# Optimization experiments

Measured on AMD Instinct MI355X. Metric: run time of the kernel, lower is better.

The kernel has to match this reference:

```python
import jax, jax.numpy as jnp
import numpy as np

B, S, H, E, T, L = 128, 1024, 512, 512, 64, 128


def setup_inputs() -> dict:
    key = jax.random.key(0)
    ks = jax.random.split(key, 20)
    s = 0.02
    inp = {
        "sent_lengths": jax.random.randint(ks[0], (B,), 1, S, dtype=jnp.int32),
        "output_length": T,
        "decoder_input": jax.random.normal(ks[1], (B, E), jnp.float32),
        "h0": jax.random.normal(ks[2], (B, H), jnp.float32),
        "c0": jax.random.normal(ks[3], (B, H), jnp.float32),
        "context": jax.random.normal(ks[4], (B, S, H), jnp.float32),
        "cur_labels": jax.random.randint(ks[5], (B, T), 0, L, dtype=jnp.int32),
        "cur_max_nsymbs": jax.random.randint(ks[6], (B,), 0, 10, dtype=jnp.int32),
        # parameters
        "label_emb": jax.random.normal(ks[7], (L, E), jnp.float32) * s,
        "W_ih": jax.random.normal(ks[8], (4 * H, E), jnp.float32) * s,
        "b_ih": jnp.zeros((4 * H,), jnp.float32),
        "W_hh": jax.random.normal(ks[9], (4 * H, H), jnp.float32) * s,
        "b_hh": jnp.zeros((4 * H,), jnp.float32),
        "W_ho": jax.random.normal(ks[10], (H, 2 * H), jnp.float32) * s,
        "b_ho": jnp.zeros((H,), jnp.float32),
        "W_attn_in": jax.random.normal(ks[11], (H, H), jnp.float32) * s,
        "b_attn_in": jnp.zeros((H,), jnp.float32),
        "W_attn_ctx": jax.random.normal(ks[12], (H, H), jnp.float32) * s,
        "b_attn_ctx": jnp.zeros((H,), jnp.float32),
        "V": jax.random.uniform(ks[13], (H,), jnp.float32, -1.0, 1.0),
        "W_out": jax.random.normal(ks[14], (L, 2 * H + E), jnp.float32) * s,
        "b_out": jnp.zeros((L,), jnp.float32),
    }
    # padding_idx row of the label embedding is zero (torch nn.Embedding semantics)
    inp["label_emb"] = inp["label_emb"].at[0].set(0.0)
    return inp


def _decode(output_length, decoder_input, h0, c0, context, cur_labels,
            label_emb, W_ih, b_ih, W_hh, b_hh, W_ho, b_ho,
            W_attn_in, b_attn_in, W_attn_ctx, b_attn_ctx, V, W_out, b_out):
    # Precompute the 1x1-conv context projection once (identical math to per-step conv).
    ctx = jnp.einsum("bsh,gh->bsg", context, W_attn_ctx) + b_attn_ctx  # [B,S,H]

    # Teacher-forced input sequence: x_0 = decoder_input, x_i = emb(labels[:, i-1]).
    emb = label_emb[cur_labels]                     # [B,T,E]
    xs = jnp.concatenate(
        [decoder_input[None], jnp.swapaxes(emb, 0, 1)[: output_length - 1]], axis=0
    )                                               # [T,B,E]

    def step(carry, x):
        h, c = carry
        gates = x @ W_ih.T + b_ih + h @ W_hh.T + b_hh          # [B,4H]
        i_g, f_g, g_g, o_g = jnp.split(gates, 4, axis=1)
        c_t = jax.nn.sigmoid(f_g) * c + jax.nn.sigmoid(i_g) * jnp.tanh(g_g)
        h_lstm = jax.nn.sigmoid(o_g) * jnp.tanh(c_t)            # [B,H]
        # pointer attention
        inp = h_lstm @ W_attn_in.T + b_attn_in                  # [B,H]
        att = jnp.einsum("bsh,h->bs", jnp.tanh(inp[:, None, :] + ctx), V)
        alpha = jax.nn.softmax(att, axis=-1)                    # [B,S]
        weighted = jnp.einsum("bs,bsh->bh", alpha, ctx)         # [B,H]
        hidden_t = jnp.tanh(jnp.concatenate([weighted, h_lstm], 1) @ W_ho.T + b_ho)
        out = jnp.concatenate([hidden_t, weighted, x], 1) @ W_out.T + b_out  # [B,L]
        return (hidden_t, c_t), out

    (h_f, c_f), outs = jax.lax.scan(step, (h0, c0), xs)  # outs [T,B,L]
    outputs = jnp.transpose(outs, (1, 0, 2))             # [B,T,L]
    preds = jnp.argmax(outputs, axis=-1)                 # [B,T]
    return outputs, preds, h_f, c_f


def reference(sent_lengths, output_length, decoder_input, h0, c0, context,
              cur_labels, cur_max_nsymbs, label_emb, W_ih, b_ih, W_hh, b_hh,
              W_ho, b_ho, W_attn_in, b_attn_in, W_attn_ctx, b_attn_ctx, V,
              W_out, b_out):
    # cur_batch_len = len(sent_lengths) == B, so hidden slicing is a no-op here.
    # cur_max_nsymbs unused (constrained_decoding=None path).
    return _decode(output_length, decoder_input, h0, c0, context, cur_labels,
                   label_emb, W_ih, b_ih, W_hh, b_hh, W_ho, b_ho,
                   W_attn_in, b_attn_in, W_attn_ctx, b_attn_ctx, V, W_out, b_out)
```

## Files before the change

### kernel.cpp

```cpp
#include <hip/hip_runtime.h>
#include <hip/hip_bf16.h>
#include <math.h>

#define B_ 128
#define S_ 1024
#define H_ 512
#define E_ 512
#define T_ 64
#define L_ 128
#define G4H 2048

__device__ inline float sigmoidf_(float x) { return 1.f / (1.f + expf(-x)); }
__device__ inline float fast_tanhf_(float x) {
    float e = __expf(2.f * x);
    return 1.f - 2.f / (e + 1.f);
}

__global__ __launch_bounds__(256) void gemm128(
    const float* __restrict__ A, int lda,
    const float* __restrict__ W, int ldw,
    const float* __restrict__ bias,
    const float* __restrict__ Cinit, int ldci,
    float* __restrict__ C, int ldc,
    int K, int act, int perm)
{
    __shared__ float As[16][128];
    __shared__ float Ws[16][128];
    const int m0 = blockIdx.x * 128;
    const int n0 = blockIdx.y * 128;
    const int t = threadIdx.x;
    const int tx = t & 15;
    const int ty = t >> 4;
    const int lr = t >> 1;
    const int lk = (t & 1) * 8;

    float acc[8][8] = {};

    for (int k0 = 0; k0 < K; k0 += 16) {
        float4 a0 = *reinterpret_cast<const float4*>(A + (size_t)(m0 + lr) * lda + k0 + lk);
        float4 a1 = *reinterpret_cast<const float4*>(A + (size_t)(m0 + lr) * lda + k0 + lk + 4);
        float4 w0 = *reinterpret_cast<const float4*>(W + (size_t)(n0 + lr) * ldw + k0 + lk);
        float4 w1 = *reinterpret_cast<const float4*>(W + (size_t)(n0 + lr) * ldw + k0 + lk + 4);
        As[lk + 0][lr] = a0.x; As[lk + 1][lr] = a0.y; As[lk + 2][lr] = a0.z; As[lk + 3][lr] = a0.w;
        As[lk + 4][lr] = a1.x; As[lk + 5][lr] = a1.y; As[lk + 6][lr] = a1.z; As[lk + 7][lr] = a1.w;
        Ws[lk + 0][lr] = w0.x; Ws[lk + 1][lr] = w0.y; Ws[lk + 2][lr] = w0.z; Ws[lk + 3][lr] = w0.w;
        Ws[lk + 4][lr] = w1.x; Ws[lk + 5][lr] = w1.y; Ws[lk + 6][lr] = w1.z; Ws[lk + 7][lr] = w1.w;
        __syncthreads();
#pragma unroll
        for (int kk = 0; kk < 16; ++kk) {
            float a[8], b[8];
#pragma unroll
            for (int i = 0; i < 8; ++i) a[i] = As[kk][ty * 8 + i];
#pragma unroll
            for (int j = 0; j < 8; ++j) b[j] = Ws[kk][tx * 8 + j];
#pragma unroll
            for (int i = 0; i < 8; ++i)
#pragma unroll
                for (int j = 0; j < 8; ++j) acc[i][j] = fmaf(a[i], b[j], acc[i][j]);
        }
        __syncthreads();
    }

#pragma unroll
    for (int i = 0; i < 8; ++i) {
        const int m = m0 + ty * 8 + i;
        size_t crow;
        if (perm) { int bb = m & 127, tt = m >> 7; crow = ((size_t)bb * T_ + tt) * ldc; }
        else crow = (size_t)m * ldc;
#pragma unroll
        for (int j = 0; j < 8; ++j) {
            const int n = n0 + tx * 8 + j;
            float v = acc[i][j];
            if (bias)  v += bias[n];
            if (Cinit) v += Cinit[(size_t)m * ldci + n];
            if (act == 1) v = tanhf(v);
            C[crow + n] = v;
        }
    }
}

__global__ __launch_bounds__(256) void gemm_stepk(
    const float* __restrict__ A, int lda,
    const float* __restrict__ W, int ldw,
    float* __restrict__ P, int N, int Kc)
{
    __shared__ float As[16][128];
    __shared__ float Ws[16][64];
    const int n0 = blockIdx.x * 64;
    const int k0 = blockIdx.y * Kc;
    const int t = threadIdx.x;
    const int tx = t & 15;
    const int ty = t >> 4;
    const int ar = t >> 1, akq = (t & 1) * 8;
    const int wr = t >> 2, wkq = (t & 3) * 4;

    float acc[8][4] = {};

    for (int kb = 0; kb < Kc; kb += 16) {
        float4 a0 = *reinterpret_cast<const float4*>(A + (size_t)ar * lda + k0 + kb + akq);
        float4 a1 = *reinterpret_cast<const float4*>(A + (size_t)ar * lda + k0 + kb + akq + 4);
        float4 w0 = *reinterpret_cast<const float4*>(W + (size_t)(n0 + wr) * ldw + k0 + kb + wkq);
        As[akq + 0][ar] = a0.x; As[akq + 1][ar] = a0.y; As[akq + 2][ar] = a0.z; As[akq + 3][ar] = a0.w;
        As[akq + 4][ar] = a1.x; As[akq + 5][ar] = a1.y; As[akq + 6][ar] = a1.z; As[akq + 7][ar] = a1.w;
        Ws[wkq + 0][wr] = w0.x; Ws[wkq + 1][wr] = w0.y; Ws[wkq + 2][wr] = w0.z; Ws[wkq + 3][wr] = w0.w;
        __syncthreads();
#pragma unroll
        for (int kk = 0; kk < 16; ++kk) {
            float a[8], b[4];
#pragma unroll
            for (int i = 0; i < 8; ++i) a[i] = As[kk][ty * 8 + i];
#pragma unroll
            for (int j = 0; j < 4; ++j) b[j] = Ws[kk][tx * 4 + j];
#pragma unroll
            for (int i = 0; i < 8; ++i)
#pragma unroll
                for (int j = 0; j < 4; ++j) acc[i][j] = fmaf(a[i], b[j], acc[i][j]);
        }
        __syncthreads();
    }

#pragma unroll
    for (int i = 0; i < 8; ++i) {
        const int m = ty * 8 + i;
#pragma unroll
        for (int j = 0; j < 4; ++j)
            P[((size_t)blockIdx.y * 128 + m) * N + n0 + tx * 4 + j] = acc[i][j];
    }
}

__global__ void k_embed(const float* __restrict__ dec_in, const int* __restrict__ labels,
                        const float* __restrict__ emb, float* __restrict__ X)
{
    size_t total = (size_t)T_ * B_ * E_;
    for (size_t i = (size_t)blockIdx.x * blockDim.x + threadIdx.x; i < total;
         i += (size_t)gridDim.x * blockDim.x) {
        int e = (int)(i % E_);
        int b = (int)((i / E_) % B_);
        int t = (int)(i / ((size_t)E_ * B_));
        float v;
        if (t == 0) v = dec_in[b * E_ + e];
        else {
            int lab = labels[b * T_ + (t - 1)];
            v = emb[(size_t)lab * E_ + e];
        }
        X[i] = v;
    }
}

__global__ void k_init(const float* __restrict__ h0, const float* __restrict__ c0,
                       const float* __restrict__ b_ih, const float* __restrict__ b_hh,
                       float* __restrict__ hbuf, float* __restrict__ cbuf, float* __restrict__ bsum)
{
    int i = blockIdx.x * blockDim.x + threadIdx.x;
    hbuf[i] = h0[i];
    cbuf[i] = c0[i];
    if (i < G4H) bsum[i] = b_ih[i] + b_hh[i];
}

__global__ __launch_bounds__(256) void k_lstm(const float* __restrict__ Pg,
                                              const float* __restrict__ xproj_t,
                                              float* __restrict__ cbuf, float* __restrict__ cat1)
{
    int i = blockIdx.x * blockDim.x + threadIdx.x;
    int b = i >> 9, h = i & 511;
    const float* p0 = Pg + (size_t)b * G4H;
    const float* p1 = Pg + (size_t)(128 + b) * G4H;
    const float* xp = xproj_t + (size_t)b * G4H;
    float ig = sigmoidf_(p0[h] + p1[h] + xp[h]);
    float fg = sigmoidf_(p0[h + 512] + p1[h + 512] + xp[h + 512]);
    float gg = tanhf(p0[h + 1024] + p1[h + 1024] + xp[h + 1024]);
    float og = sigmoidf_(p0[h + 1536] + p1[h + 1536] + xp[h + 1536]);
    float c = fg * cbuf[i] + ig * gg;
    cbuf[i] = c;
    cat1[b * 1024 + 512 + h] = og * tanhf(c);
}

__global__ __launch_bounds__(512) void k_attn(const float* __restrict__ ctx,
    const float* __restrict__ Pa, const float* __restrict__ b_ain,
    const float* __restrict__ Vv,
    float* __restrict__ pm, float* __restrict__ pl, float* __restrict__ pw)
{
    int blk = blockIdx.x;
    int b = blk >> 2, q = blk & 3;
    int tid = threadIdx.x, lane = tid & 63, wv = tid >> 6;

    __shared__ float inp_sh[512];
    inp_sh[tid] = Pa[(size_t)b * 512 + tid]
                + Pa[(size_t)(128 + b) * 512 + tid]
                + Pa[(size_t)(256 + b) * 512 + tid]
                + Pa[(size_t)(384 + b) * 512 + tid]
                + b_ain[tid];
    __syncthreads();

    float inpr[8], vr[8];
    {
        const float4* v4 = reinterpret_cast<const float4*>(Vv) + lane * 2;
        *(float4*)&vr[0] = v4[0];   *(float4*)&vr[4] = v4[1];
#pragma unroll
        for (int k = 0; k < 8; ++k) inpr[k] = inp_sh[lane * 8 + k];
    }
    const float* cbase = ctx + (size_t)b * S_ * H_ + (size_t)(q * 256) * H_;

    float m = -INFINITY, l = 0.f, w[8] = {};
    for (int si = 0; si < 32; ++si) {
        int s = wv * 32 + si;
        const float4* cp = reinterpret_cast<const float4*>(cbase + (size_t)s * H_) + lane * 2;
        float c8[8];
        *(float4*)&c8[0] = cp[0]; *(float4*)&c8[4] = cp[1];
        float t = 0.f;
#pragma unroll
        for (int k = 0; k < 8; ++k) t = fmaf(fast_tanhf_(inpr[k] + c8[k]), vr[k], t);
#pragma unroll
        for (int off = 32; off > 0; off >>= 1) t += __shfl_xor(t, off);
        float mn = fmaxf(m, t);
        float sc = __expf(m - mn);
        float p  = __expf(t - mn);
        l = l * sc + p;
#pragma unroll
        for (int k = 0; k < 8; ++k) w[k] = w[k] * sc + p * c8[k];
        m = mn;
    }

    __shared__ float wl[8 * 512];
    __shared__ float ml[8], ll[8];
#pragma unroll
    for (int k = 0; k < 8; ++k) wl[wv * 512 + lane * 8 + k] = w[k];
    if (lane == 0) { ml[wv] = m; ll[wv] = l; }
    __syncthreads();

    float M = ml[0];
#pragma unroll
    for (int u = 1; u < 8; ++u) M = fmaxf(M, ml[u]);
    float lt = 0.f, wt = 0.f;
#pragma unroll
    for (int u = 0; u < 8; ++u) {
        float e = __expf(ml[u] - M);
        lt += e * ll[u];
        wt += e * wl[u * 512 + tid];
    }
    if (tid == 0) { pm[blk] = M; pl[blk] = lt; }
    pw[(size_t)blk * 512 + tid] = wt;
}

__global__ __launch_bounds__(512) void k_merge(const float* __restrict__ pm,
    const float* __restrict__ pl, const float* __restrict__ pw,
    float* __restrict__ cat1, float* __restrict__ hist_t)
{
    int b = blockIdx.x, h = threadIdx.x;
    float M = -INFINITY;
#pragma unroll
    for (int q = 0; q < 4; ++q) M = fmaxf(M, pm[4 * b + q]);
    float L = 0.f, wt = 0.f;
#pragma unroll
    for (int q = 0; q < 4; ++q) {
        float e = __expf(pm[4 * b + q] - M);
        L += e * pl[4 * b + q];
        wt += e * pw[(size_t)(4 * b + q) * 512 + h];
    }
    float wv = wt / L;
    cat1[b * 1024 + h] = wv;
    hist_t[(size_t)b * 1024 + 512 + h] = wv;
}

__global__ __launch_bounds__(256) void k_whofin(const float* __restrict__ Po,
    const float* __restrict__ b_ho, float* __restrict__ hbuf, float* __restrict__ hist_t)
{
    int i = blockIdx.x * blockDim.x + threadIdx.x;
    int b = i >> 9, h = i & 511;
    float v = b_ho[h];
#pragma unroll
    for (int ks = 0; ks < 8; ++ks) v += Po[((size_t)ks * 128 + b) * 512 + h];
    v = tanhf(v);
    hbuf[i] = v;
    hist_t[(size_t)b * 1024 + h] = v;
}

__global__ __launch_bounds__(128) void k_argmax(const float* __restrict__ outp,
                                                float* __restrict__ preds)
{
    int row = blockIdx.x;
    int tid = threadIdx.x;
    float v = outp[(size_t)row * L_ + tid];
    int idx = tid;
#pragma unroll
    for (int off = 32; off > 0; off >>= 1) {
        float ov = __shfl_xor(v, off);
        int oi = __shfl_xor(idx, off);
        if (ov > v || (ov == v && oi < idx)) { v = ov; idx = oi; }
    }
    __shared__ float sv[2];
    __shared__ int si[2];
    if ((tid & 63) == 0) { sv[tid >> 6] = v; si[tid >> 6] = idx; }
    __syncthreads();
    if (tid == 0) {
        float v0 = sv[0], v1 = sv[1];
        int i0 = si[0], i1 = si[1];
        int r = (v1 > v0 || (v1 == v0 && i1 < i0)) ? i1 : i0;
        preds[row] = (float)r;
    }
}

__global__ void k_final(const float* __restrict__ hbuf, const float* __restrict__ cbuf,
                        float* __restrict__ hf, float* __restrict__ cf)
{
    int i = blockIdx.x * blockDim.x + threadIdx.x;
    hf[i] = hbuf[i];
    cf[i] = cbuf[i];
}

extern "C" void kernel_launch(void* const* d_in, const int* in_sizes, int n_in,
                              void* d_out, int out_size, void* d_ws, size_t ws_size,
                              hipStream_t stream)
{
    const float* dec_in  = (const float*)d_in[2];
    const float* h0      = (const float*)d_in[3];
    const float* c0      = (const float*)d_in[4];
    const float* context = (const float*)d_in[5];
    const int*   labels  = (const int*)d_in[6];
    const float* emb     = (const float*)d_in[8];
    const float* W_ih    = (const float*)d_in[9];
    const float* b_ih    = (const float*)d_in[10];
    const float* W_hh    = (const float*)d_in[11];
    const float* b_hh    = (const float*)d_in[12];
    const float* W_ho    = (const float*)d_in[13];
    const float* b_ho    = (const float*)d_in[14];
    const float* W_ain   = (const float*)d_in[15];
    const float* b_ain   = (const float*)d_in[16];
    const float* W_actx  = (const float*)d_in[17];
    const float* b_actx  = (const float*)d_in[18];
    const float* Vv      = (const float*)d_in[19];
    const float* W_out   = (const float*)d_in[20];
    const float* b_out   = (const float*)d_in[21];

    float* ws = (float*)d_ws;
    float* X     = ws; ws += (size_t)T_ * B_ * E_;
    float* xproj = ws; ws += (size_t)T_ * B_ * G4H;
    float* xout  = ws; ws += (size_t)T_ * B_ * L_;
    float* ctx   = ws; ws += (size_t)B_ * S_ * H_;
    float* hist  = ws; ws += (size_t)T_ * B_ * 1024;
    float* Pg    = ws; ws += (size_t)2 * B_ * G4H;
    float* Pa    = ws; ws += (size_t)4 * B_ * H_;
    float* Po    = ws; ws += (size_t)8 * B_ * H_;
    float* cbuf  = ws; ws += (size_t)B_ * H_;
    float* cat1  = ws; ws += (size_t)B_ * 1024;
    float* hbuf  = ws; ws += (size_t)B_ * H_;
    float* pm    = ws; ws += 512;
    float* pl    = ws; ws += 512;
    float* pw    = ws; ws += (size_t)512 * 512;
    float* bsum  = ws; ws += G4H;

    float* out_logits = (float*)d_out;
    float* out_preds  = out_logits + (size_t)B_ * T_ * L_;
    float* out_hf     = out_preds + (size_t)B_ * T_;
    float* out_cf     = out_hf + (size_t)B_ * H_;

    k_embed<<<2048, 256, 0, stream>>>(dec_in, labels, emb, X);
    k_init<<<256, 256, 0, stream>>>(h0, c0, b_ih, b_hh, hbuf, cbuf, bsum);
    gemm128<<<dim3(64, 16), 256, 0, stream>>>(X, E_, W_ih, E_, bsum, nullptr, 0,
                                              xproj, G4H, E_, 0, 0);
    gemm128<<<dim3(64, 1), 256, 0, stream>>>(X, E_, W_out + 1024, 1536, b_out, nullptr, 0,
                                             xout, L_, E_, 0, 0);
    gemm128<<<dim3(1024, 4), 256, 0, stream>>>(context, H_, W_actx, H_, b_actx, nullptr, 0,
                                               ctx, H_, H_, 0, 0);

    for (int t = 0; t < T_; ++t) {
        float* hist_t = hist + (size_t)t * B_ * 1024;
        gemm_stepk<<<dim3(32, 2), 256, 0, stream>>>(hbuf, H_, W_hh, H_, Pg, G4H, 256);
        k_lstm<<<256, 256, 0, stream>>>(Pg, xproj + (size_t)t * B_ * G4H, cbuf, cat1);
        gemm_stepk<<<dim3(8, 4), 256, 0, stream>>>(cat1 + 512, 1024, W_ain, H_, Pa, H_, 128);
        k_attn<<<512, 512, 0, stream>>>(ctx, Pa, b_ain, Vv, pm, pl, pw);
        k_merge<<<128, 512, 0, stream>>>(pm, pl, pw, cat1, hist_t);
        gemm_stepk<<<dim3(8, 8), 256, 0, stream>>>(cat1, 1024, W_ho, 1024, Po, H_, 128);
        k_whofin<<<256, 256, 0, stream>>>(Po, b_ho, hbuf, hist_t);
    }

    gemm128<<<dim3(64, 1), 256, 0, stream>>>(hist, 1024, W_out, 1536, nullptr,
                                             xout, L_, out_logits, L_, 1024, 0, 1);
    k_argmax<<<B_ * T_, 128, 0, stream>>>(out_logits, out_preds);
    k_final<<<256, 256, 0, stream>>>(hbuf, cbuf, out_hf, out_cf);
}
```

Measured before the change: 8.916 ms.

## Use split-bf16 MFMA for context projection, fuse merge with W_ho GEMV, split LSTM K

The one-time context projection GEMM moves to a bf16 MFMA kernel that splits each fp32 operand into high and low bf16 parts and uses three MFMA products to keep close to fp32 accuracy. Inside the per-step loop, the attention merge, the W_ho projection and the tanh finalize are fused into one kernel that computes a GEMV per batch pair, which removes two launches and the Po partial-sum buffer. The W_hh step GEMM's K split goes from 2 to 4 slices, and k_lstm sums four partial results. Risks include lower precision from the bf16 split and a fused GEMV of only 64 blocks, each rereading W_ho from global memory.

```diff
diff --git a/kernel.cpp b/kernel.cpp
--- a/kernel.cpp
+++ b/kernel.cpp
@@ -10,10 +10,17 @@
 #define L_ 128
 #define G4H 2048
 
+typedef __attribute__((ext_vector_type(8))) short bf16x8;
+typedef __attribute__((ext_vector_type(4))) float f32x4;
+
 __device__ inline float sigmoidf_(float x) { return 1.f / (1.f + expf(-x)); }
 __device__ inline float fast_tanhf_(float x) {
     float e = __expf(2.f * x);
     return 1.f - 2.f / (e + 1.f);
+}
+__device__ inline unsigned f2bf1(float f) {
+    unsigned u = __float_as_uint(f);
+    return (u + 0x7fffu + ((u >> 16) & 1u)) >> 16;
 }
 
 __global__ __launch_bounds__(256) void gemm128(
@@ -77,6 +84,95 @@
             C[crow + n] = v;
         }
     }
+}
+
+#define LDP 40
+__global__ __launch_bounds__(256) void gemm_ctx_split(
+    const float* __restrict__ A,
+    const float* __restrict__ W,
+    const float* __restrict__ bias,
+    float* __restrict__ C)
+{
+    __shared__ unsigned short Ah[128 * LDP];
+    __shared__ unsigned short Al[128 * LDP];
+    __shared__ unsigned short Bh[128 * LDP];
+    __shared__ unsigned short Bl[128 * LDP];
+    const int n0 = blockIdx.x * 128;
+    const int m0 = blockIdx.y * 128;
+    const int t = threadIdx.x;
+    const int lane = t & 63, wv = t >> 6;
+    const int wr = wv >> 1, wc = wv & 1;
+    const int row = t >> 1, koff = (t & 1) * 16;
+
+    f32x4 acc[4][4] = {};
+
+    for (int kt = 0; kt < 512; kt += 32) {
+        float av[16], wvv[16];
+        {
+            const float* ap = A + (size_t)(m0 + row) * 512 + kt + koff;
+            const float* wp = W + (size_t)(n0 + row) * 512 + kt + koff;
+#pragma unroll
+            for (int q = 0; q < 4; ++q) {
+                *reinterpret_cast<float4*>(&av[q * 4]) = *reinterpret_cast<const float4*>(ap + q * 4);
+                *reinterpret_cast<float4*>(&wvv[q * 4]) = *reinterpret_cast<const float4*>(wp + q * 4);
+            }
+        }
+        unsigned short ah[16], al[16], bh[16], bl[16];
+#pragma unroll
+        for (int e = 0; e < 16; ++e) {
+            unsigned ha = f2bf1(av[e]);
+            float hf = __uint_as_float(ha << 16);
+            ah[e] = (unsigned short)ha;
+            al[e] = (unsigned short)f2bf1(av[e] - hf);
+            unsigned hw = f2bf1(wvv[e]);
+            float hwf = __uint_as_float(hw << 16);
+            bh[e] = (unsigned short)hw;
+            bl[e] = (unsigned short)f2bf1(wvv[e] - hwf);
+        }
+        __syncthreads();
+        *reinterpret_cast<uint4*>(&Ah[row * LDP + koff])     = *reinterpret_cast<uint4*>(&ah[0]);
+        *reinterpret_cast<uint4*>(&Ah[row * LDP + koff + 8]) = *reinterpret_cast<uint4*>(&ah[8]);
+        *reinterpret_cast<uint4*>(&Al[row * LDP + koff])     = *reinterpret_cast<uint4*>(&al[0]);
+        *reinterpret_cast<uint4*>(&Al[row * LDP + koff + 8]) = *reinterpret_cast<uint4*>(&al[8]);
+        *reinterpret_cast<uint4*>(&Bh[row * LDP + koff])     = *reinterpret_cast<uint4*>(&bh[0]);
+        *reinterpret_cast<uint4*>(&Bh[row * LDP + koff + 8]) = *reinterpret_cast<uint4*>(&bh[8]);
+        *reinterpret_cast<uint4*>(&Bl[row * LDP + koff])     = *reinterpret_cast<uint4*>(&bl[0]);
+        *reinterpret_cast<uint4*>(&Bl[row * LDP + koff + 8]) = *reinterpret_cast<uint4*>(&bl[8]);
+        __syncthreads();
+
+        bf16x8 fah[4], fal[4], fbh[4], fbl[4];
+        const int kq = (lane >> 4) * 8;
+#pragma unroll
+        for (int i = 0; i < 4; ++i) {
+            const int ar = wr * 64 + i * 16 + (lane & 15);
+            const int br = wc * 64 + i * 16 + (lane & 15);
+            fah[i] = *reinterpret_cast<const bf16x8*>(&Ah[ar * LDP + kq]);
+            fal[i] = *reinterpret_cast<const bf16x8*>(&Al[ar * LDP + kq]);
+            fbh[i] = *reinterpret_cast<const bf16x8*>(&Bh[br * LDP + kq]);
+            fbl[i] = *reinterpret_cast<const bf16x8*>(&Bl[br * LDP + kq]);
+        }
+#pragma unroll
+        for (int i = 0; i < 4; ++i)
+#pragma unroll
+            for (int j = 0; j < 4; ++j) {
+                acc[i][j] = __builtin_amdgcn_mfma_f32_16x16x32_bf16(fah[i], fbh[j], acc[i][j], 0, 0, 0);
+                acc[i][j] = __builtin_amdgcn_mfma_f32_16x16x32_bf16(fal[i], fbh[j], acc[i][j], 0, 0, 0);
+                acc[i][j] = __builtin_amdgcn_mfma_f32_16x16x32_bf16(fah[i], fbl[j], acc[i][j], 0, 0, 0);
+            }
+    }
+
+#pragma unroll
+    for (int i = 0; i < 4; ++i)
+#pragma unroll
+        for (int j = 0; j < 4; ++j) {
+            const int n = n0 + wc * 64 + j * 16 + (lane & 15);
+            const float bs = bias[n];
+#pragma unroll
+            for (int r = 0; r < 4; ++r) {
+                const int m = m0 + wr * 64 + i * 16 + (lane >> 4) * 4 + r;
+                C[(size_t)m * 512 + n] = acc[i][j][r] + bs;
+            }
+        }
 }
 
 __global__ __launch_bounds__(256) void gemm_stepk(
@@ -165,11 +261,13 @@
     int b = i >> 9, h = i & 511;
     const float* p0 = Pg + (size_t)b * G4H;
     const float* p1 = Pg + (size_t)(128 + b) * G4H;
+    const float* p2 = Pg + (size_t)(256 + b) * G4H;
+    const float* p3 = Pg + (size_t)(384 + b) * G4H;
     const float* xp = xproj_t + (size_t)b * G4H;
-    float ig = sigmoidf_(p0[h] + p1[h] + xp[h]);
-    float fg = sigmoidf_(p0[h + 512] + p1[h + 512] + xp[h + 512]);
-    float gg = tanhf(p0[h + 1024] + p1[h + 1024] + xp[h + 1024]);
-    float og = sigmoidf_(p0[h + 1536] + p1[h + 1536] + xp[h + 1536]);
+    float ig = sigmoidf_(p0[h] + p1[h] + p2[h] + p3[h] + xp[h]);
+    float fg = sigmoidf_(p0[h + 512] + p1[h + 512] + p2[h + 512] + p3[h + 512] + xp[h + 512]);
+    float gg = tanhf(p0[h + 1024] + p1[h + 1024] + p2[h + 1024] + p3[h + 1024] + xp[h + 1024]);
+    float og = sigmoidf_(p0[h + 1536] + p1[h + 1536] + p2[h + 1536] + p3[h + 1536] + xp[h + 1536]);
     float c = fg * cbuf[i] + ig * gg;
     cbuf[i] = c;
     cat1[b * 1024 + 512 + h] = og * tanhf(c);
@@ -242,37 +340,52 @@
     pw[(size_t)blk * 512 + tid] = wt;
 }
 
-__global__ __launch_bounds__(512) void k_merge(const float* __restrict__ pm,
-    const float* __restrict__ pl, const float* __restrict__ pw,
-    float* __restrict__ cat1, float* __restrict__ hist_t)
-{
-    int b = blockIdx.x, h = threadIdx.x;
-    float M = -INFINITY;
-#pragma unroll
-    for (int q = 0; q < 4; ++q) M = fmaxf(M, pm[4 * b + q]);
-    float L = 0.f, wt = 0.f;
-#pragma unroll
-    for (int q = 0; q < 4; ++q) {
-        float e = __expf(pm[4 * b + q] - M);
-        L += e * pl[4 * b + q];
-        wt += e * pw[(size_t)(4 * b + q) * 512 + h];
-    }
-    float wv = wt / L;
-    cat1[b * 1024 + h] = wv;
-    hist_t[(size_t)b * 1024 + 512 + h] = wv;
-}
-
-__global__ __launch_bounds__(256) void k_whofin(const float* __restrict__ Po,
-    const float* __restrict__ b_ho, float* __restrict__ hbuf, float* __restrict__ hist_t)
-{
-    int i = blockIdx.x * blockDim.x + threadIdx.x;
-    int b = i >> 9, h = i & 511;
-    float v = b_ho[h];
-#pragma unroll
-    for (int ks = 0; ks < 8; ++ks) v += Po[((size_t)ks * 128 + b) * 512 + h];
-    v = tanhf(v);
-    hbuf[i] = v;
-    hist_t[(size_t)b * 1024 + h] = v;
+__global__ __launch_bounds__(512) void k_mergewho(
+    const float* __restrict__ pm, const float* __restrict__ pl,
+    const float* __restrict__ pw, const float* __restrict__ cat1,
+    const float* __restrict__ W_ho, const float* __restrict__ b_ho,
+    float* __restrict__ hbuf, float* __restrict__ hist_t)
+{
+    const int b0 = blockIdx.x * 2;
+    const int h = threadIdx.x;
+    __shared__ float catL[2][1024];
+
+#pragma unroll
+    for (int bb = 0; bb < 2; ++bb) {
+        const int b = b0 + bb;
+        float M = -INFINITY;
+#pragma unroll
+        for (int q = 0; q < 4; ++q) M = fmaxf(M, pm[4 * b + q]);
+        float L = 0.f, wt = 0.f;
+#pragma unroll
+        for (int q = 0; q < 4; ++q) {
+            float e = __expf(pm[4 * b + q] - M);
+            L += e * pl[4 * b + q];
+            wt += e * pw[(size_t)(4 * b + q) * 512 + h];
+        }
+        float wvv = wt / L;
+        catL[bb][h] = wvv;
+        catL[bb][512 + h] = cat1[(size_t)b * 1024 + 512 + h];
+        hist_t[(size_t)b * 1024 + 512 + h] = wvv;
+    }
+    __syncthreads();
+
+    float a0 = b_ho[h], a1 = a0;
+    const float4* wrow = reinterpret_cast<const float4*>(W_ho + (size_t)h * 1024);
+    for (int k4 = 0; k4 < 256; ++k4) {
+        float4 w4 = wrow[k4];
+        float4 c0 = *reinterpret_cast<const float4*>(&catL[0][k4 * 4]);
+        float4 c1 = *reinterpret_cast<const float4*>(&catL[1][k4 * 4]);
+        a0 = fmaf(w4.x, c0.x, a0); a0 = fmaf(w4.y, c0.y, a0);
+        a0 = fmaf(w4.z, c0.z, a0); a0 = fmaf(w4.w, c0.w, a0);
+        a1 = fmaf(w4.x, c1.x, a1); a1 = fmaf(w4.y, c1.y, a1);
+        a1 = fmaf(w4.z, c1.z, a1); a1 = fmaf(w4.w, c1.w, a1);
+    }
+    float v0 = tanhf(a0), v1 = tanhf(a1);
+    hbuf[(size_t)b0 * 512 + h] = v0;
+    hbuf[(size_t)(b0 + 1) * 512 + h] = v1;
+    hist_t[(size_t)b0 * 1024 + h] = v0;
+    hist_t[(size_t)(b0 + 1) * 1024 + h] = v1;
 }
 
 __global__ __launch_bounds__(128) void k_argmax(const float* __restrict__ outp,
@@ -338,9 +451,8 @@
     float* xout  = ws; ws += (size_t)T_ * B_ * L_;
     float* ctx   = ws; ws += (size_t)B_ * S_ * H_;
     float* hist  = ws; ws += (size_t)T_ * B_ * 1024;
-    float* Pg    = ws; ws += (size_t)2 * B_ * G4H;
+    float* Pg    = ws; ws += (size_t)4 * B_ * G4H;
     float* Pa    = ws; ws += (size_t)4 * B_ * H_;
-    float* Po    = ws; ws += (size_t)8 * B_ * H_;
     float* cbuf  = ws; ws += (size_t)B_ * H_;
     float* cat1  = ws; ws += (size_t)B_ * 1024;
     float* hbuf  = ws; ws += (size_t)B_ * H_;
@@ -360,18 +472,15 @@
                                               xproj, G4H, E_, 0, 0);
     gemm128<<<dim3(64, 1), 256, 0, stream>>>(X, E_, W_out + 1024, 1536, b_out, nullptr, 0,
                                              xout, L_, E_, 0, 0);
-    gemm128<<<dim3(1024, 4), 256, 0, stream>>>(context, H_, W_actx, H_, b_actx, nullptr, 0,
-                                               ctx, H_, H_, 0, 0);
+    gemm_ctx_split<<<dim3(4, 1024), 256, 0, stream>>>(context, W_actx, b_actx, ctx);
 
     for (int t = 0; t < T_; ++t) {
         float* hist_t = hist + (size_t)t * B_ * 1024;
-        gemm_stepk<<<dim3(32, 2), 256, 0, stream>>>(hbuf, H_, W_hh, H_, Pg, G4H, 256);
+        gemm_stepk<<<dim3(32, 4), 256, 0, stream>>>(hbuf, H_, W_hh, H_, Pg, G4H, 128);
         k_lstm<<<256, 256, 0, stream>>>(Pg, xproj + (size_t)t * B_ * G4H, cbuf, cat1);
         gemm_stepk<<<dim3(8, 4), 256, 0, stream>>>(cat1 + 512, 1024, W_ain, H_, Pa, H_, 128);
         k_attn<<<512, 512, 0, stream>>>(ctx, Pa, b_ain, Vv, pm, pl, pw);
-        k_merge<<<128, 512, 0, stream>>>(pm, pl, pw, cat1, hist_t);
-        gemm_stepk<<<dim3(8, 8), 256, 0, stream>>>(cat1, 1024, W_ho, 1024, Po, H_, 128);
-        k_whofin<<<256, 256, 0, stream>>>(Po, b_ho, hbuf, hist_t);
+        k_mergewho<<<64, 512, 0, stream>>>(pm, pl, pw, cat1, W_ho, b_ho, hbuf, hist_t);
     }
 
     gemm128<<<dim3(64, 1), 256, 0, stream>>>(hist, 1024, W_out, 1536, nullptr,
```

After: 10.28 ms. +15.3%, slower.
